# Optimization experiments

Hardware: AMD Instinct MI355X
Metric: run time of the kernel (lower is better)

The kernel has to match this reference:

```python
import jax, jax.numpy as jnp
import numpy as np

N_NODES = 100000
N_EDGES = 1600000


def setup_inputs() -> dict:
    key = jax.random.key(0)
    ks = jax.random.split(key, 6)
    x = jax.random.normal(ks[0], (N_NODES, 128), dtype=jnp.float32)
    edge_src = jax.random.randint(ks[1], (N_EDGES,), 0, N_NODES, dtype=jnp.int64)
    edge_dst = jax.random.randint(ks[2], (N_EDGES,), 0, N_NODES, dtype=jnp.int64)
    # GCNConv weights (bias=False); glorot-like scaling
    W1 = jax.random.normal(ks[3], (128, 64), dtype=jnp.float32) * (1.0 / np.sqrt(128))
    W2 = jax.random.normal(ks[4], (64, 64), dtype=jnp.float32) * (1.0 / np.sqrt(64))
    W3 = jax.random.normal(ks[5], (64, 40), dtype=jnp.float32) * (1.0 / np.sqrt(64))
    return {"x": x, "edge_src": edge_src, "edge_dst": edge_dst,
            "W1": W1, "W2": W2, "W3": W3}


def reference(x, edge_src, edge_dst, W1, W2, W3):
    # SGC forward (eval mode: dropout is identity).
    # Each GCNConv(normalize=False, bias=False): out = A @ (h @ W)
    n = x.shape[0]

    def conv(h, W):
        hw = h @ W                      # [N, d_out] dense transform
        msgs = hw[edge_src]             # [E, d_out] gather over edges
        return jax.ops.segment_sum(msgs, edge_dst, num_segments=n)  # scatter-add

    h = conv(x, W1)
    h = conv(h, W2)
    h = conv(h, W3)
    return jax.nn.log_softmax(h, axis=-1)
```

## Files before the change

### kernel.cpp

```cpp
#include <hip/hip_runtime.h>
#include <hip/hip_fp16.h>
#include <math.h>


#define BW    128
#define NBMAX 1024
#define BCAP  3072
#define D     40
#define RS    64
#define NPW   12
#define PCHUNK 4096

typedef unsigned short u16;
typedef unsigned int   u32;

static __device__ inline u32 hadd2u(u32 a, u32 b) {
    __half2 ha = *(__half2*)&a, hb = *(__half2*)&b;
    __half2 r = __hadd2(ha, hb);
    return *(u32*)&r;
}

__global__ void k_w12(const float* __restrict__ W1, const float* __restrict__ W2,
                      float* __restrict__ W12, int* __restrict__ gcnt) {
    int idx = blockIdx.x * blockDim.x + threadIdx.x;
    if (blockIdx.x == 0) {
        for (int i = threadIdx.x; i < NBMAX; i += blockDim.x) gcnt[i] = 0;
    }
    if (idx >= 128 * 64) return;
    int r = idx >> 6, c = idx & 63;
    float acc = 0.f;
#pragma unroll
    for (int k = 0; k < 64; ++k) acc += W1[r * 64 + k] * W2[k * 64 + c];
    W12[idx] = acc;
}

__global__ void k_wc(const float* __restrict__ W12, const float* __restrict__ W3,
                     float* __restrict__ Wc) {
    int idx = blockIdx.x * blockDim.x + threadIdx.x;
    if (idx >= 128 * 40) return;
    int r = idx / 40, c = idx - r * 40;
    float acc = 0.f;
#pragma unroll
    for (int k = 0; k < 64; ++k) acc += W12[r * 64 + k] * W3[k * 40 + c];
    Wc[idx] = acc;
}

__global__ void k_gp(const float4* __restrict__ x4, const float4* __restrict__ Wc4,
                     u16* __restrict__ yout, int n_nodes,
                     const int* __restrict__ src, const int* __restrict__ dst,
                     int* __restrict__ gcnt, int* __restrict__ part,
                     int E, int nb, int npart) {
    __shared__ union {
        struct { int h[NBMAX]; int base[NBMAX]; } p;
        float4 wc[1280];
    } sm;
    int t = threadIdx.x;

    if ((int)blockIdx.x < npart) {
        int e0 = blockIdx.x * PCHUNK;
        int e1 = min(e0 + PCHUNK, E);
        for (int i = t; i < nb; i += 256) sm.p.h[i] = 0;
        __syncthreads();
        for (int e = e0 + t; e < e1; e += 1024) {
#pragma unroll
            for (int u = 0; u < 4; ++u) {
                int ee = e + u * 256;
                if (ee < e1) atomicAdd(&sm.p.h[dst[ee] >> 7], 1);
            }
        }
        __syncthreads();
        for (int i = t; i < nb; i += 256) {
            int c = sm.p.h[i];
            sm.p.base[i] = c ? atomicAdd(&gcnt[i], c) : 0;
        }
        __syncthreads();
        for (int i = t; i < nb; i += 256) sm.p.h[i] = 0;
        __syncthreads();
        for (int eb = e0 + t; eb < e1; eb += 2048) {
            int dd[8], ss[8], pp[8];
#pragma unroll
            for (int u = 0; u < 8; ++u) {
                int e = eb + u * 256;
                bool v = e < e1;
                dd[u] = v ? dst[e] : 0;
                ss[u] = v ? src[e] : 0;
            }
#pragma unroll
            for (int u = 0; u < 8; ++u) {
                int e = eb + u * 256;
                int b = dd[u] >> 7;
                pp[u] = (e < e1) ? (sm.p.base[b] + atomicAdd(&sm.p.h[b], 1)) : BCAP;
            }
#pragma unroll
            for (int u = 0; u < 8; ++u) {
                int b = dd[u] >> 7;
                if (pp[u] < BCAP)
                    part[(size_t)b * BCAP + pp[u]] = (ss[u] << 7) | (dd[u] & 127);
            }
        }
    } else {
        for (int i = t; i < 1280; i += 256) sm.wc[i] = Wc4[i];
        __syncthreads();
        int tid = ((int)blockIdx.x - npart) * 256 + t;
        int node = tid / 5, j0 = tid - node * 5;
        if (node >= n_nodes) return;
        float4 a0 = {0.f, 0.f, 0.f, 0.f}, a1 = {0.f, 0.f, 0.f, 0.f};
        const float4* xr = x4 + (size_t)node * 32;
#pragma unroll
        for (int k4 = 0; k4 < 32; ++k4) {
            float4 v = xr[k4];
#pragma unroll
            for (int kk = 0; kk < 4; ++kk) {
                float c = (kk == 0) ? v.x : (kk == 1) ? v.y : (kk == 2) ? v.z : v.w;
                float4 w0 = sm.wc[(k4 * 4 + kk) * 10 + j0 * 2];
                float4 w1 = sm.wc[(k4 * 4 + kk) * 10 + j0 * 2 + 1];
                a0.x += c * w0.x; a0.y += c * w0.y; a0.z += c * w0.z; a0.w += c * w0.w;
                a1.x += c * w1.x; a1.y += c * w1.y; a1.z += c * w1.z; a1.w += c * w1.w;
            }
        }
        __half2 h0 = __floats2half2_rn(a0.x, a0.y);
        __half2 h1 = __floats2half2_rn(a0.z, a0.w);
        __half2 h2 = __floats2half2_rn(a1.x, a1.y);
        __half2 h3 = __floats2half2_rn(a1.z, a1.w);
        uint4 st;
        st.x = *(u32*)&h0; st.y = *(u32*)&h1; st.z = *(u32*)&h2; st.w = *(u32*)&h3;
        *(uint4*)(yout + (size_t)node * RS + j0 * 8) = st;
    }
}

__global__ void k_csr(const int* __restrict__ part, const int* __restrict__ gcnt,
                      int2* __restrict__ offs2, int* __restrict__ ssort, int N) {
    __shared__ int cnt[BW];
    __shared__ int pos[BW];
    __shared__ int cur[BW];
    __shared__ int wsum[2];
    int b = blockIdx.x, t = threadIdx.x;
    int m = min(gcnt[b], BCAP);
    const int* bp = part + (size_t)b * BCAP;
    if (t < BW) cnt[t] = 0;
    __syncthreads();
    for (int k = t; k < m; k += 256)
        atomicAdd(&cnt[bp[k] & 127], 1);
    __syncthreads();
    int v = 0, inc = 0;
    if (t < BW) {
        v = cnt[t];
        inc = v;
#pragma unroll
        for (int off = 1; off < 64; off <<= 1) {
            int u = __shfl_up(inc, off, 64);
            if ((t & 63) >= off) inc += u;
        }
        if ((t & 63) == 63) wsum[t >> 6] = inc;
    }
    __syncthreads();
    int node0 = b * BW;
    if (t < BW) {
        int local = ((t >= 64) ? wsum[0] : 0) + inc - v;
        pos[t] = local;
        cur[t] = 0;
        if (node0 + t < N)
            offs2[node0 + t] = make_int2(b * BCAP + local, b * BCAP + local + v);
    }
    __syncthreads();
    for (int k = t; k < m; k += 256) {
        int p = bp[k];
        int r = p & 127;
        int loc = atomicAdd(&cur[r], 1);
        ssort[(size_t)b * BCAP + pos[r] + loc] = p >> 7;
    }
}

template <int FINAL>
__global__ void k_agg(const u16* __restrict__ yin, void* __restrict__ youtv,
                      const int2* __restrict__ offs2, const int* __restrict__ srcs,
                      int n_nodes) {
    int wid = (blockIdx.x * blockDim.x + threadIdx.x) >> 6;
    int lane = threadIdx.x & 63;
    int g = lane / 5;
    int sub = lane - g * 5;
    int node = wid * NPW + g;
    bool nv = (g < NPW) && (node < n_nodes);
    int2 be = offs2[nv ? node : 0];
    int beg = be.x;
    int deg = nv ? (be.y - be.x) : 0;
    u32 suboff = (u32)sub * 16u;
    u32 c0 = 0, c1 = 0, c2 = 0, c3 = 0;
    u32 d0 = 0, d1 = 0, d2 = 0, d3 = 0;
    int mdeg = deg;
#pragma unroll
    for (int off = 1; off < 64; off <<= 1)
        mdeg = max(mdeg, __shfl_xor(mdeg, off, 64));
    int sv0 = (sub < deg) ? srcs[beg + sub] : 0;
    int sv1 = (5 + sub < deg) ? srcs[beg + 5 + sub] : 0;
    for (int k = 0; k < mdeg; k += 10) {
        int kn = k + 10;
        int svn0 = (kn + sub < deg) ? srcs[beg + kn + sub] : 0;
        int svn1 = (kn + 5 + sub < deg) ? srcs[beg + kn + 5 + sub] : 0;
#pragma unroll
        for (int j = 0; j < 5; ++j) {
            int s = __shfl(sv0, g * 5 + j, 64);
            if (k + j < deg) {
                uint4 w = *(const uint4*)((const char*)yin +
                              (size_t)(((u32)s << 7) + suboff));
                c0 = hadd2u(c0, w.x); c1 = hadd2u(c1, w.y);
                c2 = hadd2u(c2, w.z); c3 = hadd2u(c3, w.w);
            }
        }
#pragma unroll
        for (int j = 0; j < 5; ++j) {
            int s = __shfl(sv1, g * 5 + j, 64);
            if (k + 5 + j < deg) {
                uint4 w = *(const uint4*)((const char*)yin +
                              (size_t)(((u32)s << 7) + suboff));
                d0 = hadd2u(d0, w.x); d1 = hadd2u(d1, w.y);
                d2 = hadd2u(d2, w.z); d3 = hadd2u(d3, w.w);
            }
        }
        sv0 = svn0; sv1 = svn1;
    }
    c0 = hadd2u(c0, d0); c1 = hadd2u(c1, d1);
    c2 = hadd2u(c2, d2); c3 = hadd2u(c3, d3);
    if (FINAL) {
        float2 f0 = __half22float2(*(__half2*)&c0);
        float2 f1 = __half22float2(*(__half2*)&c1);
        float2 f2 = __half22float2(*(__half2*)&c2);
        float2 f3 = __half22float2(*(__half2*)&c3);
        int s1 = sub + 1; s1 = (s1 >= 5) ? s1 - 5 : s1;
        int s2 = sub + 2; s2 = (s2 >= 5) ? s2 - 5 : s2;
        int s4 = sub + 4; s4 = (s4 >= 5) ? s4 - 5 : s4;
        int r1 = g * 5 + s1, r2 = g * 5 + s2, r4 = g * 5 + s4;
        float m0 = fmaxf(fmaxf(fmaxf(f0.x, f0.y), fmaxf(f1.x, f1.y)),
                         fmaxf(fmaxf(f2.x, f2.y), fmaxf(f3.x, f3.y)));
        float m = fmaxf(m0, __shfl(m0, r1, 64));
        m = fmaxf(m, __shfl(m, r2, 64));
        m = fmaxf(m, __shfl(m0, r4, 64));
        float e0 = __expf(f0.x - m) + __expf(f0.y - m) + __expf(f1.x - m) +
                   __expf(f1.y - m) + __expf(f2.x - m) + __expf(f2.y - m) +
                   __expf(f3.x - m) + __expf(f3.y - m);
        float sm = e0 + __shfl(e0, r1, 64);
        sm = sm + __shfl(sm, r2, 64);
        sm = sm + __shfl(e0, r4, 64);
        float ls = __logf(sm) + m;
        if (nv) {
            float4 o1 = {f0.x - ls, f0.y - ls, f1.x - ls, f1.y - ls};
            float4 o2 = {f2.x - ls, f2.y - ls, f3.x - ls, f3.y - ls};
            float* op = (float*)youtv + (size_t)node * D + sub * 8;
            *(float4*)op = o1;
            *(float4*)(op + 4) = o2;
        }
    } else {
        if (nv) {
            uint4 st = {c0, c1, c2, c3};
            *(uint4*)((u16*)youtv + (size_t)node * RS + sub * 8) = st;
        }
    }
}

extern "C" void kernel_launch(void* const* d_in, const int* in_sizes, int n_in,
                              void* d_out, int out_size, void* d_ws, size_t ws_size,
                              hipStream_t stream) {
    const float* x   = (const float*)d_in[0];
    const int* esrc  = (const int*)d_in[1];
    const int* edst  = (const int*)d_in[2];
    const float* W1  = (const float*)d_in[3];
    const float* W2  = (const float*)d_in[4];
    const float* W3  = (const float*)d_in[5];
    int N = in_sizes[0] / 128;
    int E = in_sizes[1];
    float* out = (float*)d_out;

    int nb = (N + BW - 1) / BW;

    char* ws = (char*)d_ws;
    auto alloc = [&](size_t bytes) {
        char* p = ws;
        ws += (bytes + 255) & ~(size_t)255;
        return p;
    };
    u16* bufA   = (u16*)alloc((size_t)N * RS * sizeof(u16));
    u16* bufB   = (u16*)alloc((size_t)N * RS * sizeof(u16));
    int* part   = (int*)bufB;
    int* ssort  = (int*)alloc((size_t)nb * BCAP * sizeof(int));
    int2* offs2 = (int2*)alloc((size_t)N * sizeof(int2));
    float* W12  = (float*)alloc(128 * 64 * sizeof(float));
    float* Wc   = (float*)alloc(128 * 40 * sizeof(float));
    int* gcnt   = (int*)alloc(NBMAX * sizeof(int));

    k_w12<<<(128 * 64 + 255) / 256, 256, 0, stream>>>(W1, W2, W12, gcnt);
    k_wc<<<(128 * 40 + 255) / 256, 256, 0, stream>>>(W12, W3, Wc);

    int npart = (E + PCHUNK - 1) / PCHUNK;
    int ngemm = (N * 5 + 255) / 256;
    k_gp<<<npart + ngemm, 256, 0, stream>>>((const float4*)x, (const float4*)Wc,
                                            bufA, N, esrc, edst, gcnt, part,
                                            E, nb, npart);

    k_csr<<<nb, 256, 0, stream>>>(part, gcnt, offs2, ssort, N);

    int nwaves = (N + NPW - 1) / NPW;
    int agg_grid = (nwaves + 3) / 4;
    k_agg<0><<<agg_grid, 256, 0, stream>>>(bufA, bufB, offs2, ssort, N);
    k_agg<0><<<agg_grid, 256, 0, stream>>>(bufB, bufA, offs2, ssort, N);
    k_agg<1><<<agg_grid, 256, 0, stream>>>(bufA, out, offs2, ssort, N);
}
```

Baseline: 165.2 us.

## Sort nodes by degree before aggregation to balance wave work

Builds a degree histogram inside the CSR kernel, scans it, and scatters each node's edge range and id into degree-sorted order. The aggregation kernels then process nodes in that order, so the 12 nodes sharing a wave have similar degree and the wave loop, bounded by the wave's maximum degree, wastes fewer iterations. The cost is two extra small kernel launches, extra arrays, and outputs written in scattered rather than contiguous node order.

New measurement: 174.4 us. +5.6%, slower.

```diff
diff --git a/kernel.cpp b/kernel.cpp
--- a/kernel.cpp
+++ b/kernel.cpp
@@ -10,6 +10,7 @@
 #define RS    64
 #define NPW   12
 #define PCHUNK 4096
+#define DBINS 128
 
 typedef unsigned short u16;
 typedef unsigned int   u32;
@@ -21,10 +22,12 @@
 }
 
 __global__ void k_w12(const float* __restrict__ W1, const float* __restrict__ W2,
-                      float* __restrict__ W12, int* __restrict__ gcnt) {
+                      float* __restrict__ W12, int* __restrict__ gcnt,
+                      int* __restrict__ dcnt) {
     int idx = blockIdx.x * blockDim.x + threadIdx.x;
     if (blockIdx.x == 0) {
         for (int i = threadIdx.x; i < NBMAX; i += blockDim.x) gcnt[i] = 0;
+        if (threadIdx.x < DBINS) dcnt[threadIdx.x] = 0;
     }
     if (idx >= 128 * 64) return;
     int r = idx >> 6, c = idx & 63;
@@ -129,15 +132,18 @@
 }
 
 __global__ void k_csr(const int* __restrict__ part, const int* __restrict__ gcnt,
-                      int2* __restrict__ offs2, int* __restrict__ ssort, int N) {
+                      int2* __restrict__ offs2, int* __restrict__ ssort,
+                      int* __restrict__ dcnt, int N) {
     __shared__ int cnt[BW];
     __shared__ int pos[BW];
     __shared__ int cur[BW];
     __shared__ int wsum[2];
+    __shared__ int dh[DBINS];
     int b = blockIdx.x, t = threadIdx.x;
     int m = min(gcnt[b], BCAP);
     const int* bp = part + (size_t)b * BCAP;
     if (t < BW) cnt[t] = 0;
+    if (t >= BW && t < BW + DBINS) dh[t - BW] = 0;
     __syncthreads();
     for (int k = t; k < m; k += 256)
         atomicAdd(&cnt[bp[k] & 127], 1);
@@ -159,10 +165,13 @@
         int local = ((t >= 64) ? wsum[0] : 0) + inc - v;
         pos[t] = local;
         cur[t] = 0;
-        if (node0 + t < N)
+        if (node0 + t < N) {
             offs2[node0 + t] = make_int2(b * BCAP + local, b * BCAP + local + v);
-    }
-    __syncthreads();
+            atomicAdd(&dh[min(v, DBINS - 1)], 1);
+        }
+    }
+    __syncthreads();
+    if (t < DBINS && dh[t]) atomicAdd(&dcnt[t], dh[t]);
     for (int k = t; k < m; k += 256) {
         int p = bp[k];
         int r = p & 127;
@@ -171,17 +180,71 @@
     }
 }
 
+__global__ void k_dscan(const int* __restrict__ dcnt, int* __restrict__ dcur) {
+    __shared__ int sh[DBINS];
+    int t = threadIdx.x;
+    int v = dcnt[t];
+    sh[t] = v;
+    __syncthreads();
+    for (int off = 1; off < DBINS; off <<= 1) {
+        int u = (t >= off) ? sh[t - off] : 0;
+        __syncthreads();
+        sh[t] += u;
+        __syncthreads();
+    }
+    dcur[t] = sh[t] - v;
+}
+
+__global__ void k_dscat(const int2* __restrict__ offs2, int* __restrict__ dcur,
+                        int2* __restrict__ sbe, int* __restrict__ snode, int N) {
+    __shared__ int h[DBINS];
+    __shared__ int base[DBINS];
+    int t = threadIdx.x;
+    int n0 = blockIdx.x * 1024;
+    int n1 = min(n0 + 1024, N);
+    if (t < DBINS) h[t] = 0;
+    __syncthreads();
+    int2 be[4]; int bin[4];
+#pragma unroll
+    for (int u = 0; u < 4; ++u) {
+        int n = n0 + t + u * 256;
+        bin[u] = -1;
+        if (n < n1) {
+            be[u] = offs2[n];
+            bin[u] = min(be[u].y - be[u].x, DBINS - 1);
+            atomicAdd(&h[bin[u]], 1);
+        }
+    }
+    __syncthreads();
+    if (t < DBINS) {
+        int c = h[t];
+        base[t] = c ? atomicAdd(&dcur[t], c) : 0;
+        h[t] = 0;
+    }
+    __syncthreads();
+#pragma unroll
+    for (int u = 0; u < 4; ++u) {
+        if (bin[u] >= 0) {
+            int p = base[bin[u]] + atomicAdd(&h[bin[u]], 1);
+            sbe[p] = be[u];
+            snode[p] = n0 + t + u * 256;
+        }
+    }
+}
+
 template <int FINAL>
 __global__ void k_agg(const u16* __restrict__ yin, void* __restrict__ youtv,
-                      const int2* __restrict__ offs2, const int* __restrict__ srcs,
-                      int n_nodes) {
+                      const int2* __restrict__ sbe, const int* __restrict__ snode,
+                      const int* __restrict__ srcs, int n_nodes) {
     int wid = (blockIdx.x * blockDim.x + threadIdx.x) >> 6;
     int lane = threadIdx.x & 63;
     int g = lane / 5;
     int sub = lane - g * 5;
-    int node = wid * NPW + g;
-    bool nv = (g < NPW) && (node < n_nodes);
-    int2 be = offs2[nv ? node : 0];
+    int item = wid * NPW + g;
+    bool nv = (g < NPW) && (item < n_nodes);
+    int cl = nv ? item : 0;
+    int2 be = sbe[cl];
+    int node = snode[cl];
     int beg = be.x;
     int deg = nv ? (be.y - be.x) : 0;
     u32 suboff = (u32)sub * 16u;
@@ -283,11 +346,15 @@
     int* part   = (int*)bufB;
     int* ssort  = (int*)alloc((size_t)nb * BCAP * sizeof(int));
     int2* offs2 = (int2*)alloc((size_t)N * sizeof(int2));
+    int2* sbe   = (int2*)alloc((size_t)N * sizeof(int2));
+    int* snode  = (int*)alloc((size_t)N * sizeof(int));
     float* W12  = (float*)alloc(128 * 64 * sizeof(float));
     float* Wc   = (float*)alloc(128 * 40 * sizeof(float));
     int* gcnt   = (int*)alloc(NBMAX * sizeof(int));
-
-    k_w12<<<(128 * 64 + 255) / 256, 256, 0, stream>>>(W1, W2, W12, gcnt);
+    int* dcnt   = (int*)alloc(DBINS * sizeof(int));
+    int* dcur   = (int*)alloc(DBINS * sizeof(int));
+
+    k_w12<<<(128 * 64 + 255) / 256, 256, 0, stream>>>(W1, W2, W12, gcnt, dcnt);
     k_wc<<<(128 * 40 + 255) / 256, 256, 0, stream>>>(W12, W3, Wc);
 
     int npart = (E + PCHUNK - 1) / PCHUNK;
@@ -296,11 +363,13 @@
                                             bufA, N, esrc, edst, gcnt, part,
                                             E, nb, npart);
 
-    k_csr<<<nb, 256, 0, stream>>>(part, gcnt, offs2, ssort, N);
+    k_csr<<<nb, 256, 0, stream>>>(part, gcnt, offs2, ssort, dcnt, N);
+    k_dscan<<<1, DBINS, 0, stream>>>(dcnt, dcur);
+    k_dscat<<<(N + 1023) / 1024, 256, 0, stream>>>(offs2, dcur, sbe, snode, N);
 
     int nwaves = (N + NPW - 1) / NPW;
     int agg_grid = (nwaves + 3) / 4;
-    k_agg<0><<<agg_grid, 256, 0, stream>>>(bufA, bufB, offs2, ssort, N);
-    k_agg<0><<<agg_grid, 256, 0, stream>>>(bufB, bufA, offs2, ssort, N);
-    k_agg<1><<<agg_grid, 256, 0, stream>>>(bufA, out, offs2, ssort, N);
-}
+    k_agg<0><<<agg_grid, 256, 0, stream>>>(bufA, bufB, sbe, snode, ssort, N);
+    k_agg<0><<<agg_grid, 256, 0, stream>>>(bufB, bufA, sbe, snode, ssort, N);
+    k_agg<1><<<agg_grid, 256, 0, stream>>>(bufA, out, sbe, snode, ssort, N);
+}
```
